# Kernel tuning notes

Hardware: AMD Instinct MI355X
Metric: run time of the kernel (lower is better)

Reference implementation:

```python
import jax, jax.numpy as jnp
import numpy as np

DR = 0.1
L = 24.0
N_FRAMES = 16
N_ATOMS = 512


def setup_inputs() -> dict:
    key = jax.random.key(0)
    # coordinates uniform in the periodic box [0, L)^3
    traj = jax.random.uniform(key, (N_FRAMES, N_ATOMS, 3), dtype=jnp.float32) * L
    cell = jnp.eye(3, dtype=jnp.float32) * L
    # r_list = arange(0.5*dr, L_max - 2*dr, dr) with L_max = cell[0,0]/2 -> 118 bins
    r_list = jnp.arange(0.5 * DR, L / 2 - 2 * DR, DR, dtype=jnp.float32)
    return {"traj": traj, "cell": cell, "r_list": r_list}


def _frame_hist(q, cell_diag, r_list, cutoff_sq):
    # q: [N,3]; dense minimum-image pairwise displacements, upper-triangle pairs only
    disp = q[None, :, :] - q[:, None, :]                        # [N,N,3]
    offsets = jax.lax.stop_gradient(jnp.floor(disp / cell_diag + 0.5))
    disp = disp - offsets * cell_diag                           # minimum image
    sq = jnp.sum(disp * disp, axis=-1)                          # [N,N]
    n = q.shape[0]
    triu = jnp.triu(jnp.ones((n, n), dtype=bool))               # torch.triu zeros lower part
    sq = jnp.where(triu, sq, 0.0)
    mask = (sq < cutoff_sq) & (sq != 0.0)                       # i<j and within cutoff
    d = jnp.sqrt(jnp.where(mask, sq, 1.0))                      # safe sqrt (masked out below)
    centered = d[:, :, None] - r_list[None, None, :]            # [N,N,B]
    g = (1.0 / (DR * np.sqrt(2.0 * np.pi))) * jnp.exp(-0.5 * (centered / DR) ** 2)
    g = g * mask[:, :, None].astype(g.dtype)                    # drop excluded pairs (== nonzero extraction)
    return g.sum(axis=(0, 1)) * DR                              # [B]


def reference(traj, cell, r_list):
    cell_diag = jnp.diag(cell)                                  # [3]
    cutoff_sq = (cell[0, 0] / 2.0) ** 2                         # L_max = cell[0,0]/2 (default)

    def step(acc, q):
        return acc + _frame_hist(q, cell_diag, r_list, cutoff_sq), None

    hist0 = jnp.zeros(r_list.shape, dtype=traj.dtype)
    hist, _ = jax.lax.scan(step, hist0, traj)                   # accumulate over frames like the python loop
    hist = hist / traj.shape[0]

    v = (4.0 * np.pi / 3.0) * ((r_list + 0.5 * DR) ** 3 - (r_list - 0.5 * DR) ** 3)
    natom = traj.shape[1]
    det = jnp.linalg.det(cell)
    gr = hist / v * det / (natom - 1) / natom * 2.0
    return (r_list, gr)
```

## Files before the change

### kernel.cpp

```cpp
#include <hip/hip_runtime.h>
#include <math.h>

#define N_ATOMS 512
#define MAX_B 128
#define NBUCK 32
#define WIN 0.65f

__global__ void zero_kernel(float* p, int n) {
    int t = blockIdx.x * blockDim.x + threadIdx.x;
    if (t < n) p[t] = 0.0f;
}

__global__ __launch_bounds__(256) void pair_kernel(
    const float* __restrict__ traj, const float* __restrict__ cell,
    const float* __restrict__ r_list, float* __restrict__ part,
    int B, int atomic_mode)
{
    __shared__ float qx[N_ATOMS], qy[N_ATOMS], qz[N_ATOMS];
    __shared__ float dsorted[2048];
    __shared__ int   cnt[NBUCK];
    __shared__ int   start[NBUCK + 1];
    __shared__ int   cursor[NBUCK];
    __shared__ float accbuf[256];

    const int frame = blockIdx.x >> 6;
    const int sub   = blockIdx.x & 63;
    const int tid   = threadIdx.x;

    const float* q = traj + (size_t)frame * (N_ATOMS * 3);
    for (int a = tid; a < N_ATOMS; a += 256) {
        qx[a] = q[3 * a + 0];
        qy[a] = q[3 * a + 1];
        qz[a] = q[3 * a + 2];
    }
    if (tid < NBUCK) cnt[tid] = 0;
    __syncthreads();

    const float L = cell[0];
    const float invL = 1.0f / L;
    const float cutoff_sq = 0.25f * L * L;
    const float inv_bw = (float)NBUCK / (0.5f * L);

    float dval[8];
    int   dbuck[8];
    #pragma unroll
    for (int s = 0; s < 8; ++s) {
        const int qidx = s * 256 + tid;
        const int rp   = sub * 4 + (qidx >> 9);
        const int qq   = qidx & 511;
        const int lenA = 511 - rp;
        const bool inA = qq < lenA;
        const int i = inA ? rp : (510 - rp);
        const int j = inA ? (rp + 1 + qq) : qq;
        const bool vp = !(rp == 255 && !inA);

        float dx = qx[j] - qx[i];
        float dy = qy[j] - qy[i];
        float dz = qz[j] - qz[i];
        dx -= L * floorf(dx * invL + 0.5f);
        dy -= L * floorf(dy * invL + 0.5f);
        dz -= L * floorf(dz * invL + 0.5f);
        const float d2 = dx * dx + dy * dy + dz * dz;

        dbuck[s] = -1;
        dval[s]  = 0.0f;
        if (vp && d2 < cutoff_sq && d2 != 0.0f) {
            const float d = sqrtf(d2);
            int b = (int)(d * inv_bw);
            if (b > NBUCK - 1) b = NBUCK - 1;
            dval[s]  = d;
            dbuck[s] = b;
            atomicAdd(&cnt[b], 1);
        }
    }
    __syncthreads();

    if (tid < NBUCK) {
        const int v = cnt[tid];
        int incl = v;
        #pragma unroll
        for (int off = 1; off < NBUCK; off <<= 1) {
            const int n = __shfl_up(incl, off, 64);
            if (tid >= off) incl += n;
        }
        start[tid + 1] = incl;
        cursor[tid] = incl - v;
        if (tid == 0) start[0] = 0;
    }
    __syncthreads();

    #pragma unroll
    for (int s = 0; s < 8; ++s) {
        if (dbuck[s] >= 0) {
            const int pos = atomicAdd(&cursor[dbuck[s]], 1);
            dsorted[pos] = dval[s];
        }
    }
    __syncthreads();

    const int k = tid & 127;
    const int g = tid >> 7;
    float acc = 0.0f;
    if (k < B) {
        const float rk = r_list[k];
        const float c1 = -50.0f;
        const float c2 = 100.0f * rk;
        const float c3 = -50.0f * rk * rk;
        int blo = (int)(fmaxf((rk - WIN) * inv_bw, 0.0f));
        int bhi = (int)((rk + WIN) * inv_bw);
        if (bhi > NBUCK - 1) bhi = NBUCK - 1;
        const int lo = start[blo];
        const int hi = start[bhi + 1];
        for (int idx = lo + g; idx < hi; idx += 2) {
            const float d = dsorted[idx];
            acc += __expf(fmaf(d, fmaf(c1, d, c2), c3));
        }
    }
    accbuf[tid] = acc;
    __syncthreads();

    if (tid < 128) {
        const float v = accbuf[tid] + accbuf[tid + 128];
        if (atomic_mode) atomicAdd(&part[(blockIdx.x & 15) * MAX_B + tid], v);
        else             part[(size_t)blockIdx.x * MAX_B + tid] = v;
    }
}

__global__ __launch_bounds__(256) void finalize_kernel(
    const float* __restrict__ r_list, const float* __restrict__ cell,
    const float* __restrict__ part, float* __restrict__ out,
    int B, int F, int nrows)
{
    __shared__ float red[256];
    const int k = blockIdx.x;
    if (k >= B) return;

    float s = 0.0f;
    for (int t = threadIdx.x; t < nrows; t += 256) s += part[(size_t)t * MAX_B + k];
    red[threadIdx.x] = s;
    __syncthreads();
    for (int off = 128; off > 0; off >>= 1) {
        if (threadIdx.x < off) red[threadIdx.x] += red[threadIdx.x + off];
        __syncthreads();
    }
    if (threadIdx.x == 0) {
        const float r = r_list[k];
        out[k] = r;
        const float det = cell[0] * cell[4] * cell[8];
        const float rp = r + 0.05f;
        const float rm = r - 0.05f;
        const float v = (4.0f * (float)M_PI / 3.0f) * (rp * rp * rp - rm * rm * rm);
        const float inv_sqrt2pi = 0.3989422804014327f;
        const float h = red[0] * inv_sqrt2pi / (float)F;
        const float gr = h / v * det / (float)(N_ATOMS - 1) / (float)N_ATOMS * 2.0f;
        out[B + k] = gr;
    }
}

extern "C" void kernel_launch(void* const* d_in, const int* in_sizes, int n_in,
                              void* d_out, int out_size, void* d_ws, size_t ws_size,
                              hipStream_t stream) {
    const float* traj   = (const float*)d_in[0];
    const float* cell   = (const float*)d_in[1];
    const float* r_list = (const float*)d_in[2];
    float* out  = (float*)d_out;
    float* part = (float*)d_ws;

    const int B = in_sizes[2];
    const int F = in_sizes[0] / (N_ATOMS * 3);
    const int nblocks = F * 64;

    const bool partials_fit =
        ws_size >= (size_t)nblocks * MAX_B * sizeof(float);

    if (partials_fit) {
        hipLaunchKernelGGL(pair_kernel, dim3(nblocks), dim3(256), 0, stream,
                           traj, cell, r_list, part, B, 0);
        hipLaunchKernelGGL(finalize_kernel, dim3(MAX_B), dim3(256), 0, stream,
                           r_list, cell, part, out, B, F, nblocks);
    } else {
        hipLaunchKernelGGL(zero_kernel, dim3(8), dim3(256), 0, stream,
                           part, 16 * MAX_B);
        hipLaunchKernelGGL(pair_kernel, dim3(nblocks), dim3(256), 0, stream,
                           traj, cell, r_list, part, B, 1);
        hipLaunchKernelGGL(finalize_kernel, dim3(MAX_B), dim3(256), 0, stream,
                           r_list, cell, part, out, B, F, 16);
    }
}
```

Before: 77.30 us.

## Replace per-pair Gaussian evaluation with binned Taylor moment accumulation

Each pair distance is now binned into 768 fine sub-bins, and the block accumulates five power moments of the offset from the bin centre using shared-memory atomics. This replaces the per-block bucket sort and the per-r exp loop. A new reduce kernel collapses the per-block moment arrays into 32 chunks. The finalize kernel then evaluates the Gaussian per sub-bin through a 4th-order Taylor expansion, removing most exp calls. The cost is five float atomics per pair, much larger partial buffers (3840 floats per block), an extra kernel launch, and an approximation error from the truncated expansion.

New measurement: 124.4 us. 60.9% more time.

```diff
diff --git a/kernel.cpp b/kernel.cpp
--- a/kernel.cpp
+++ b/kernel.cpp
@@ -2,9 +2,12 @@
 #include <math.h>
 
 #define N_ATOMS 512
-#define MAX_B 128
-#define NBUCK 32
-#define WIN 0.65f
+#define NSUB 768
+#define NMOM 5
+#define NM (NMOM * NSUB)
+#define RCHUNK 32
+#define WIN_EVAL 0.75f
+#define NB_MAX 128
 
 __global__ void zero_kernel(float* p, int n) {
     int t = blockIdx.x * blockDim.x + threadIdx.x;
@@ -13,15 +16,11 @@
 
 __global__ __launch_bounds__(256) void pair_kernel(
     const float* __restrict__ traj, const float* __restrict__ cell,
-    const float* __restrict__ r_list, float* __restrict__ part,
-    int B, int atomic_mode)
+    float* __restrict__ part, int atomic_mode)
 {
-    __shared__ float qx[N_ATOMS], qy[N_ATOMS], qz[N_ATOMS];
-    __shared__ float dsorted[2048];
-    __shared__ int   cnt[NBUCK];
-    __shared__ int   start[NBUCK + 1];
-    __shared__ int   cursor[NBUCK];
-    __shared__ float accbuf[256];
+    __shared__ float2 qxy[N_ATOMS];
+    __shared__ float  qzs[N_ATOMS];
+    __shared__ float  M[NM];
 
     const int frame = blockIdx.x >> 6;
     const int sub   = blockIdx.x & 63;
@@ -29,20 +28,18 @@
 
     const float* q = traj + (size_t)frame * (N_ATOMS * 3);
     for (int a = tid; a < N_ATOMS; a += 256) {
-        qx[a] = q[3 * a + 0];
-        qy[a] = q[3 * a + 1];
-        qz[a] = q[3 * a + 2];
-    }
-    if (tid < NBUCK) cnt[tid] = 0;
+        qxy[a] = make_float2(q[3 * a + 0], q[3 * a + 1]);
+        qzs[a] = q[3 * a + 2];
+    }
+    for (int i = tid; i < NM; i += 256) M[i] = 0.0f;
     __syncthreads();
 
     const float L = cell[0];
     const float invL = 1.0f / L;
     const float cutoff_sq = 0.25f * L * L;
-    const float inv_bw = (float)NBUCK / (0.5f * L);
-
-    float dval[8];
-    int   dbuck[8];
+    const float inv_delta = (2.0f * (float)NSUB) / L;
+    const float delta = L / (2.0f * (float)NSUB);
+
     #pragma unroll
     for (int s = 0; s < 8; ++s) {
         const int qidx = s * 256 + tid;
@@ -54,102 +51,119 @@
         const int j = inA ? (rp + 1 + qq) : qq;
         const bool vp = !(rp == 255 && !inA);
 
-        float dx = qx[j] - qx[i];
-        float dy = qy[j] - qy[i];
-        float dz = qz[j] - qz[i];
+        const float2 pj = qxy[j];
+        const float2 pi = qxy[i];
+        float dx = pj.x - pi.x;
+        float dy = pj.y - pi.y;
+        float dz = qzs[j] - qzs[i];
         dx -= L * floorf(dx * invL + 0.5f);
         dy -= L * floorf(dy * invL + 0.5f);
         dz -= L * floorf(dz * invL + 0.5f);
         const float d2 = dx * dx + dy * dy + dz * dz;
 
-        dbuck[s] = -1;
-        dval[s]  = 0.0f;
         if (vp && d2 < cutoff_sq && d2 != 0.0f) {
             const float d = sqrtf(d2);
-            int b = (int)(d * inv_bw);
-            if (b > NBUCK - 1) b = NBUCK - 1;
-            dval[s]  = d;
-            dbuck[s] = b;
-            atomicAdd(&cnt[b], 1);
+            int b = (int)(d * inv_delta);
+            if (b > NSUB - 1) b = NSUB - 1;
+            const float eps = fmaf(-((float)b + 0.5f), delta, d);
+            const float e2 = eps * eps;
+            atomicAdd(&M[b],            1.0f);
+            atomicAdd(&M[NSUB + b],     eps);
+            atomicAdd(&M[2 * NSUB + b], e2);
+            atomicAdd(&M[3 * NSUB + b], e2 * eps);
+            atomicAdd(&M[4 * NSUB + b], e2 * e2);
         }
     }
     __syncthreads();
 
-    if (tid < NBUCK) {
-        const int v = cnt[tid];
-        int incl = v;
-        #pragma unroll
-        for (int off = 1; off < NBUCK; off <<= 1) {
-            const int n = __shfl_up(incl, off, 64);
-            if (tid >= off) incl += n;
-        }
-        start[tid + 1] = incl;
-        cursor[tid] = incl - v;
-        if (tid == 0) start[0] = 0;
-    }
-    __syncthreads();
-
-    #pragma unroll
-    for (int s = 0; s < 8; ++s) {
-        if (dbuck[s] >= 0) {
-            const int pos = atomicAdd(&cursor[dbuck[s]], 1);
-            dsorted[pos] = dval[s];
-        }
-    }
-    __syncthreads();
-
-    const int k = tid & 127;
-    const int g = tid >> 7;
-    float acc = 0.0f;
-    if (k < B) {
-        const float rk = r_list[k];
-        const float c1 = -50.0f;
-        const float c2 = 100.0f * rk;
-        const float c3 = -50.0f * rk * rk;
-        int blo = (int)(fmaxf((rk - WIN) * inv_bw, 0.0f));
-        int bhi = (int)((rk + WIN) * inv_bw);
-        if (bhi > NBUCK - 1) bhi = NBUCK - 1;
-        const int lo = start[blo];
-        const int hi = start[bhi + 1];
-        for (int idx = lo + g; idx < hi; idx += 2) {
-            const float d = dsorted[idx];
-            acc += __expf(fmaf(d, fmaf(c1, d, c2), c3));
-        }
-    }
-    accbuf[tid] = acc;
-    __syncthreads();
-
-    if (tid < 128) {
-        const float v = accbuf[tid] + accbuf[tid + 128];
-        if (atomic_mode) atomicAdd(&part[(blockIdx.x & 15) * MAX_B + tid], v);
-        else             part[(size_t)blockIdx.x * MAX_B + tid] = v;
-    }
+    if (atomic_mode) {
+        float* dst = part + (size_t)(blockIdx.x & 15) * NM;
+        for (int i = tid; i < NM; i += 256) atomicAdd(&dst[i], M[i]);
+    } else {
+        float* dst = part + (size_t)blockIdx.x * NM;
+        for (int i = tid; i < NM; i += 256) dst[i] = M[i];
+    }
+}
+
+__global__ __launch_bounds__(256) void reduce_kernel(
+    const float* __restrict__ part, float* __restrict__ part2, int nblocks)
+{
+    const int c = blockIdx.x & (RCHUNK - 1);
+    const int g = blockIdx.x / RCHUNK;
+    const int o = g * 256 + threadIdx.x;
+    const int rpc = (nblocks + RCHUNK - 1) / RCHUNK;
+    const int b0 = c * rpc;
+    float s = 0.0f;
+    for (int i = 0; i < rpc; ++i) {
+        const int b = b0 + i;
+        if (b < nblocks) s += part[(size_t)b * NM + o];
+    }
+    part2[(size_t)c * NM + o] = s;
 }
 
 __global__ __launch_bounds__(256) void finalize_kernel(
     const float* __restrict__ r_list, const float* __restrict__ cell,
-    const float* __restrict__ part, float* __restrict__ out,
+    const float* __restrict__ partR, float* __restrict__ out,
     int B, int F, int nrows)
 {
+    __shared__ float Mred[NMOM * NB_MAX];
     __shared__ float red[256];
     const int k = blockIdx.x;
     if (k >= B) return;
-
-    float s = 0.0f;
-    for (int t = threadIdx.x; t < nrows; t += 256) s += part[(size_t)t * MAX_B + k];
-    red[threadIdx.x] = s;
+    const int tid = threadIdx.x;
+
+    const float r = r_list[k];
+    const float L = cell[0];
+    const float inv_delta = (2.0f * (float)NSUB) / L;
+    const float delta = L / (2.0f * (float)NSUB);
+
+    int blo = (int)((r - WIN_EVAL) * inv_delta);
+    if (blo < 0) blo = 0;
+    int bhi = (int)((r + WIN_EVAL) * inv_delta);
+    if (bhi > NSUB - 1) bhi = NSUB - 1;
+    int nb = bhi - blo + 1;
+    if (nb > NB_MAX) nb = NB_MAX;
+
+    for (int o = tid; o < NMOM * nb; o += 256) {
+        const int m = o / nb;
+        const int bo = o - m * nb;
+        float ssum = 0.0f;
+        for (int ch = 0; ch < nrows; ++ch)
+            ssum += partR[(size_t)ch * NM + m * NSUB + blo + bo];
+        Mred[o] = ssum;
+    }
+    __syncthreads();
+
+    float acc = 0.0f;
+    if (tid < nb) {
+        const int b = blo + tid;
+        const float m0 = Mred[tid];
+        const float m1 = Mred[nb + tid];
+        const float m2 = Mred[2 * nb + tid];
+        const float m3 = Mred[3 * nb + tid];
+        const float m4 = Mred[4 * nb + tid];
+        const float u  = fmaf((float)b + 0.5f, delta, -r);
+        const float u2 = u * u;
+        const float t  = __expf(-50.0f * u2);
+        float ssum = m0;
+        ssum = fmaf(m1, -100.0f * u, ssum);
+        ssum = fmaf(m2, fmaf(5000.0f, u2, -50.0f), ssum);
+        ssum = fmaf(m3, u * fmaf(-166666.671875f, u2, 5000.0f), ssum);
+        ssum = fmaf(m4, fmaf(u2, fmaf(4166666.75f, u2, -250000.0f), 1250.0f), ssum);
+        acc = t * ssum;
+    }
+    red[tid] = acc;
     __syncthreads();
     for (int off = 128; off > 0; off >>= 1) {
-        if (threadIdx.x < off) red[threadIdx.x] += red[threadIdx.x + off];
+        if (tid < off) red[tid] += red[tid + off];
         __syncthreads();
     }
-    if (threadIdx.x == 0) {
-        const float r = r_list[k];
+    if (tid == 0) {
         out[k] = r;
         const float det = cell[0] * cell[4] * cell[8];
-        const float rp = r + 0.05f;
-        const float rm = r - 0.05f;
-        const float v = (4.0f * (float)M_PI / 3.0f) * (rp * rp * rp - rm * rm * rm);
+        const float rpv = r + 0.05f;
+        const float rmv = r - 0.05f;
+        const float v = (4.0f * (float)M_PI / 3.0f) * (rpv * rpv * rpv - rmv * rmv * rmv);
         const float inv_sqrt2pi = 0.3989422804014327f;
         const float h = red[0] * inv_sqrt2pi / (float)F;
         const float gr = h / v * det / (float)(N_ATOMS - 1) / (float)N_ATOMS * 2.0f;
@@ -170,20 +184,22 @@
     const int F = in_sizes[0] / (N_ATOMS * 3);
     const int nblocks = F * 64;
 
-    const bool partials_fit =
-        ws_size >= (size_t)nblocks * MAX_B * sizeof(float);
-
-    if (partials_fit) {
+    const size_t need = ((size_t)nblocks + RCHUNK) * NM * sizeof(float);
+
+    if (ws_size >= need) {
+        float* part2 = part + (size_t)nblocks * NM;
         hipLaunchKernelGGL(pair_kernel, dim3(nblocks), dim3(256), 0, stream,
-                           traj, cell, r_list, part, B, 0);
-        hipLaunchKernelGGL(finalize_kernel, dim3(MAX_B), dim3(256), 0, stream,
-                           r_list, cell, part, out, B, F, nblocks);
+                           traj, cell, part, 0);
+        hipLaunchKernelGGL(reduce_kernel, dim3(RCHUNK * (NM / 256)), dim3(256), 0, stream,
+                           part, part2, nblocks);
+        hipLaunchKernelGGL(finalize_kernel, dim3(B), dim3(256), 0, stream,
+                           r_list, cell, part2, out, B, F, RCHUNK);
     } else {
-        hipLaunchKernelGGL(zero_kernel, dim3(8), dim3(256), 0, stream,
-                           part, 16 * MAX_B);
+        hipLaunchKernelGGL(zero_kernel, dim3((16 * NM + 255) / 256), dim3(256), 0, stream,
+                           part, 16 * NM);
         hipLaunchKernelGGL(pair_kernel, dim3(nblocks), dim3(256), 0, stream,
-                           traj, cell, r_list, part, B, 1);
-        hipLaunchKernelGGL(finalize_kernel, dim3(MAX_B), dim3(256), 0, stream,
+                           traj, cell, part, 1);
+        hipLaunchKernelGGL(finalize_kernel, dim3(B), dim3(256), 0, stream,
                            r_list, cell, part, out, B, F, 16);
     }
 }
```

## Refine distance buckets, narrow Gaussian window, pack xy coords, unroll accumulation loop

Applied to the files above, without the earlier changes.

Doubles the number of distance buckets and shrinks the Gaussian window from 0.65 to 0.45 (4.5 sigma), so each bin scans fewer sorted distances. It also packs the x and y coordinates into float2 in shared memory so each pair needs fewer LDS loads, and unrolls the exp-accumulation loop by two with independent accumulators to expose more ILP. The narrower window drops Gaussian tail contributions beyond 4.5 sigma, which adds a small accuracy change.

After: 70.00 us. -9.4%, faster.

```diff
diff --git a/kernel.cpp b/kernel.cpp
--- a/kernel.cpp
+++ b/kernel.cpp
@@ -3,8 +3,8 @@
 
 #define N_ATOMS 512
 #define MAX_B 128
-#define NBUCK 32
-#define WIN 0.65f
+#define NBUCK 64
+#define WIN 0.45f
 
 __global__ void zero_kernel(float* p, int n) {
     int t = blockIdx.x * blockDim.x + threadIdx.x;
@@ -16,12 +16,13 @@
     const float* __restrict__ r_list, float* __restrict__ part,
     int B, int atomic_mode)
 {
-    __shared__ float qx[N_ATOMS], qy[N_ATOMS], qz[N_ATOMS];
-    __shared__ float dsorted[2048];
-    __shared__ int   cnt[NBUCK];
-    __shared__ int   start[NBUCK + 1];
-    __shared__ int   cursor[NBUCK];
-    __shared__ float accbuf[256];
+    __shared__ float2 qxy[N_ATOMS];
+    __shared__ float  qzs[N_ATOMS];
+    __shared__ float  dsorted[2048];
+    __shared__ int    cnt[NBUCK];
+    __shared__ int    start[NBUCK + 1];
+    __shared__ int    cursor[NBUCK];
+    __shared__ float  accbuf[256];
 
     const int frame = blockIdx.x >> 6;
     const int sub   = blockIdx.x & 63;
@@ -29,9 +30,8 @@
 
     const float* q = traj + (size_t)frame * (N_ATOMS * 3);
     for (int a = tid; a < N_ATOMS; a += 256) {
-        qx[a] = q[3 * a + 0];
-        qy[a] = q[3 * a + 1];
-        qz[a] = q[3 * a + 2];
+        qxy[a] = make_float2(q[3 * a + 0], q[3 * a + 1]);
+        qzs[a] = q[3 * a + 2];
     }
     if (tid < NBUCK) cnt[tid] = 0;
     __syncthreads();
@@ -54,9 +54,11 @@
         const int j = inA ? (rp + 1 + qq) : qq;
         const bool vp = !(rp == 255 && !inA);
 
-        float dx = qx[j] - qx[i];
-        float dy = qy[j] - qy[i];
-        float dz = qz[j] - qz[i];
+        const float2 pj = qxy[j];
+        const float2 pi = qxy[i];
+        float dx = pj.x - pi.x;
+        float dy = pj.y - pi.y;
+        float dz = qzs[j] - qzs[i];
         dx -= L * floorf(dx * invL + 0.5f);
         dy -= L * floorf(dy * invL + 0.5f);
         dz -= L * floorf(dz * invL + 0.5f);
@@ -111,10 +113,23 @@
         if (bhi > NBUCK - 1) bhi = NBUCK - 1;
         const int lo = start[blo];
         const int hi = start[bhi + 1];
-        for (int idx = lo + g; idx < hi; idx += 2) {
-            const float d = dsorted[idx];
-            acc += __expf(fmaf(d, fmaf(c1, d, c2), c3));
-        }
+        int idx = lo + g;
+        int nn = hi - idx;
+        nn = (nn > 0) ? ((nn + 1) >> 1) : 0;
+        float acc1 = 0.0f;
+        int m = nn >> 1;
+        while (m-- > 0) {
+            const float d0 = dsorted[idx];
+            const float d1 = dsorted[idx + 2];
+            idx += 4;
+            acc  += __expf(fmaf(d0, fmaf(c1, d0, c2), c3));
+            acc1 += __expf(fmaf(d1, fmaf(c1, d1, c2), c3));
+        }
+        if (nn & 1) {
+            const float d0 = dsorted[idx];
+            acc += __expf(fmaf(d0, fmaf(c1, d0, c2), c3));
+        }
+        acc += acc1;
     }
     accbuf[tid] = acc;
     __syncthreads();
```
